# Kernel tuning notes

Measured on AMD Instinct MI355X. Metric: run time of the kernel, lower is better.

## Reference

```python
import jax, jax.numpy as jnp
import numpy as np

N = 50000
E = 800000
N_IN = 256
N_HID = 128
N_OUT = 64
HOP = 10


def setup_inputs() -> dict:
    key = jax.random.key(0)
    ks = jax.random.split(key, 12)
    x = jax.random.normal(ks[0], (N, N_IN), dtype=jnp.float32)
    s = jax.random.randint(ks[1], (E,), 0, N, dtype=jnp.int32)
    t = jax.random.randint(ks[2], (E,), 0, N, dtype=jnp.int32)
    # parameters (xavier-ish scaling)
    fc1W = jax.random.normal(ks[3], (N_HID, N_IN), dtype=jnp.float32) * (1.0 / np.sqrt(N_IN))
    fc1b = jnp.zeros((N_HID,), dtype=jnp.float32)
    fcsW = jax.random.normal(ks[4], (HOP, N_HID, N_HID), dtype=jnp.float32) * (1.0 / np.sqrt(N_HID))
    fcsb = jnp.zeros((HOP, N_HID), dtype=jnp.float32)
    a1 = jax.random.normal(ks[5], (HOP, N_HID), dtype=jnp.float32) * (1.0 / np.sqrt(N_HID))
    a2 = jax.random.normal(ks[6], (HOP, N_HID), dtype=jnp.float32) * (1.0 / np.sqrt(N_HID))
    fc2W = jax.random.normal(ks[7], (N_OUT, N_HID), dtype=jnp.float32) * (1.0 / np.sqrt(N_HID))
    fc2b = jnp.zeros((N_OUT,), dtype=jnp.float32)
    return {"x": x, "s": s, "t": t, "fc1W": fc1W, "fc1b": fc1b,
            "fcsW": fcsW, "fcsb": fcsb, "a1": a1, "a2": a2,
            "fc2W": fc2W, "fc2b": fc2b}


def reference(x, s, t, fc1W, fc1b, fcsW, fcsb, a1, a2, fc2W, fc2b):
    # dropout layers are identity in eval mode
    x = jax.nn.relu(x @ fc1W.T + fc1b)  # [N, n_hid]
    h = x
    for i in range(HOP):
        W, b = fcsW[i], fcsb[i]
        x_new = x @ W.T + b          # [N, n_hid]
        h = h @ W.T + b              # [N, n_hid]
        x1 = x_new @ a1[i]           # [N]
        h1 = h @ a2[i]               # [N]
        w1 = jnp.exp(jax.nn.leaky_relu(x1[s] + h1[t], 0.2))       # [E]
        w2 = jnp.exp(jax.nn.leaky_relu(x1 + x_new @ a2[i], 0.2))  # [N]
        div = jax.ops.segment_sum(w1, s, num_segments=N) + w2     # [N]
        num = jax.ops.segment_sum(w1[:, None] * h[t], s, num_segments=N) + w2[:, None] * x_new
        h = jax.nn.elu(num / div[:, None])
    return h @ fc2W.T + fc2b  # [N, n_out]
```

## Files before the change

kernel.cpp:

```cpp
#include <hip/hip_runtime.h>
#include <math.h>


typedef __attribute__((ext_vector_type(8))) short short8;
typedef __attribute__((ext_vector_type(4))) float f32x4;
#define MFMA16 __builtin_amdgcn_mfma_f32_16x16x32_bf16

__device__ __forceinline__ float lrelu02(float v) { return v > 0.f ? v : 0.2f * v; }

__device__ __forceinline__ float2 bf2f2(unsigned int v) {
    return make_float2(__uint_as_float(v << 16), __uint_as_float(v & 0xffff0000u));
}
__device__ __forceinline__ unsigned int f2bf(float f) {
    unsigned int u = __float_as_uint(f);
    u += 0x7fffu + ((u >> 16) & 1u);
    return u >> 16;
}
__device__ __forceinline__ float hi_part(float f) {
    return __uint_as_float(__float_as_uint(f) & 0xffff0000u);
}
__device__ __forceinline__ uint4 pack_hi(const float4& a, const float4& b) {
    uint4 r;
    r.x = (__float_as_uint(a.x) >> 16) | (__float_as_uint(a.y) & 0xffff0000u);
    r.y = (__float_as_uint(a.z) >> 16) | (__float_as_uint(a.w) & 0xffff0000u);
    r.z = (__float_as_uint(b.x) >> 16) | (__float_as_uint(b.y) & 0xffff0000u);
    r.w = (__float_as_uint(b.z) >> 16) | (__float_as_uint(b.w) & 0xffff0000u);
    return r;
}
__device__ __forceinline__ uint4 pack_lo(const float4& a, const float4& b) {
    uint4 r;
    r.x = f2bf(a.x - hi_part(a.x)) | (f2bf(a.y - hi_part(a.y)) << 16);
    r.y = f2bf(a.z - hi_part(a.z)) | (f2bf(a.w - hi_part(a.w)) << 16);
    r.z = f2bf(b.x - hi_part(b.x)) | (f2bf(b.y - hi_part(b.y)) << 16);
    r.w = f2bf(b.z - hi_part(b.z)) | (f2bf(b.w - hi_part(b.w)) << 16);
    return r;
}

__global__ __launch_bounds__(256) void k_count(const int* __restrict__ s, int* __restrict__ cnt, int E) {
    int e = blockIdx.x * 256 + threadIdx.x;
    if (e < E) atomicAdd(&cnt[s[e]], 1);
}

__global__ __launch_bounds__(256) void k_scan1(const int* __restrict__ cnt, int* __restrict__ bs, int N) {
    __shared__ int sh[256];
    int idx = blockIdx.x * 256 + threadIdx.x;
    sh[threadIdx.x] = (idx < N) ? cnt[idx] : 0;
    __syncthreads();
#pragma unroll
    for (int off = 128; off; off >>= 1) {
        if (threadIdx.x < off) sh[threadIdx.x] += sh[threadIdx.x + off];
        __syncthreads();
    }
    if (threadIdx.x == 0) bs[blockIdx.x] = sh[0];
}

__global__ __launch_bounds__(256) void k_scan2(int* __restrict__ bs, int G) {
    __shared__ int sh[256];
    int t = threadIdx.x;
    int v = (t < G) ? bs[t] : 0;
    sh[t] = v;
    __syncthreads();
    int val = v;
#pragma unroll
    for (int off = 1; off < 256; off <<= 1) {
        int o = (t >= off) ? sh[t - off] : 0;
        __syncthreads();
        val += o; sh[t] = val;
        __syncthreads();
    }
    if (t < G) bs[t] = val - v;
}

__global__ __launch_bounds__(256) void k_scan3(const int* __restrict__ cnt, const int* __restrict__ bs,
                                               int* __restrict__ rp, int N) {
    __shared__ int sh[256];
    int t = threadIdx.x;
    int idx = blockIdx.x * 256 + t;
    int v = (idx < N) ? cnt[idx] : 0;
    sh[t] = v;
    __syncthreads();
    int val = v;
#pragma unroll
    for (int off = 1; off < 256; off <<= 1) {
        int o = (t >= off) ? sh[t - off] : 0;
        __syncthreads();
        val += o; sh[t] = val;
        __syncthreads();
    }
    if (idx <= N) rp[idx] = val - v + bs[blockIdx.x];
}

__global__ __launch_bounds__(256) void k_scatter(const int* __restrict__ s, const int* __restrict__ t,
                                                 const int* __restrict__ rp, int* __restrict__ cursor,
                                                 int* __restrict__ t_sorted, int E) {
    int e = blockIdx.x * 256 + threadIdx.x;
    if (e < E) {
        int u = s[e];
        int pos = atomicAdd(&cursor[u], 1);
        t_sorted[rp[u] + pos] = t[e];
    }
}

__global__ __launch_bounds__(256) void k_wsplit(const float* __restrict__ W,
                                                unsigned short* __restrict__ Whi,
                                                unsigned short* __restrict__ Wlo, int total) {
    int i = blockIdx.x * 256 + threadIdx.x;
    if (i < total) {
        float f = W[i];
        unsigned int u = __float_as_uint(f);
        Whi[i] = (unsigned short)(u >> 16);
        Wlo[i] = (unsigned short)f2bf(f - __uint_as_float(u & 0xffff0000u));
    }
}

__global__ __launch_bounds__(256) void k_fc1(
    const float* __restrict__ Xf,
    const unsigned short* __restrict__ Wh, const unsigned short* __restrict__ Wl,
    const float* __restrict__ bias,
    unsigned short* __restrict__ Yhi, unsigned short* __restrict__ Ylo, int N) {
    const int tid = threadIdx.x;
    const int r0 = blockIdx.x * 128;
    const int lane = tid & 63;
    const int w = tid >> 6;
    const int wr = (w >> 1) * 64, wc = (w & 1) * 64;
    const int frow = lane & 15;
    const int fk = lane >> 4;
    const int q4 = lane >> 4;

    f32x4 acc[4][4];
#pragma unroll
    for (int i = 0; i < 4; ++i)
#pragma unroll
        for (int j = 0; j < 4; ++j) acc[i][j] = (f32x4){0.f, 0.f, 0.f, 0.f};

    const float4 z4 = make_float4(0.f, 0.f, 0.f, 0.f);
#pragma unroll
    for (int kc = 0; kc < 8; ++kc) {
        short8 ah[4], al[4];
#pragma unroll
        for (int ri = 0; ri < 4; ++ri) {
            int row = r0 + wr + ri * 16 + frow;
            float4 va = z4, vb = z4;
            if (row < N) {
                const float* p = Xf + (size_t)row * 256 + kc * 32 + fk * 8;
                va = *(const float4*)p;
                vb = *(const float4*)(p + 4);
            }
            uint4 h = pack_hi(va, vb);
            uint4 l = pack_lo(va, vb);
            ah[ri] = *(short8*)&h;
            al[ri] = *(short8*)&l;
        }
#pragma unroll
        for (int ci = 0; ci < 4; ++ci) {
            int col = wc + ci * 16 + frow;
            short8 bh = *(const short8*)(Wh + (size_t)col * 256 + kc * 32 + fk * 8);
            short8 bl = *(const short8*)(Wl + (size_t)col * 256 + kc * 32 + fk * 8);
#pragma unroll
            for (int ri = 0; ri < 4; ++ri) {
                acc[ri][ci] = MFMA16(ah[ri], bh, acc[ri][ci], 0, 0, 0);
                acc[ri][ci] = MFMA16(ah[ri], bl, acc[ri][ci], 0, 0, 0);
                acc[ri][ci] = MFMA16(al[ri], bh, acc[ri][ci], 0, 0, 0);
            }
        }
    }

#pragma unroll
    for (int ci = 0; ci < 4; ++ci) {
        int col = wc + ci * 16 + frow;
        float bcol = bias[col];
#pragma unroll
        for (int ri = 0; ri < 4; ++ri) {
            f32x4 v = acc[ri][ci];
#pragma unroll
            for (int reg = 0; reg < 4; ++reg) {
                int grow = r0 + wr + ri * 16 + q4 * 4 + reg;
                if (grow < N) {
                    float val = fmaxf(v[reg] + bcol, 0.f);
                    Yhi[(size_t)grow * 128 + col] = (unsigned short)(__float_as_uint(val) >> 16);
                    Ylo[(size_t)grow * 128 + col] = (unsigned short)f2bf(val - hi_part(val));
                }
            }
        }
    }
}

__global__ __launch_bounds__(256) void k_fc2(
    const unsigned short* __restrict__ Xhi,
    const unsigned short* __restrict__ Wh, const unsigned short* __restrict__ Wl,
    const float* __restrict__ bias, float* __restrict__ Yf, int N) {
    const int tid = threadIdx.x;
    const int r0 = blockIdx.x * 64;
    const int lane = tid & 63;
    const int w = tid >> 6;
    const int wr = w * 16;
    const int frow = lane & 15;
    const int fk = lane >> 4;
    const int q4 = lane >> 4;

    f32x4 acc[4];
#pragma unroll
    for (int j = 0; j < 4; ++j) acc[j] = (f32x4){0.f, 0.f, 0.f, 0.f};

    const short8 z8 = (short8){0, 0, 0, 0, 0, 0, 0, 0};
#pragma unroll
    for (int kc = 0; kc < 4; ++kc) {
        int row = r0 + wr + frow;
        short8 ah = (row < N) ? *(const short8*)(Xhi + (size_t)row * 128 + kc * 32 + fk * 8) : z8;
#pragma unroll
        for (int ci = 0; ci < 4; ++ci) {
            int col = ci * 16 + frow;
            short8 bh = *(const short8*)(Wh + (size_t)col * 128 + kc * 32 + fk * 8);
            short8 bl = *(const short8*)(Wl + (size_t)col * 128 + kc * 32 + fk * 8);
            acc[ci] = MFMA16(ah, bh, acc[ci], 0, 0, 0);
            acc[ci] = MFMA16(ah, bl, acc[ci], 0, 0, 0);
        }
    }

#pragma unroll
    for (int ci = 0; ci < 4; ++ci) {
        int col = ci * 16 + frow;
        float bcol = bias[col];
#pragma unroll
        for (int reg = 0; reg < 4; ++reg) {
            int grow = r0 + wr + q4 * 4 + reg;
            if (grow < N) Yf[(size_t)grow * 64 + col] = acc[ci][reg] + bcol;
        }
    }
}

__global__ __launch_bounds__(256) void k_mm_bf(
    const unsigned short* __restrict__ Xhi0, const unsigned short* __restrict__ Xlo0, int nblk0,
    const unsigned short* __restrict__ Hhi1,
    const unsigned short* __restrict__ Whi, const unsigned short* __restrict__ Wlo,
    const float* __restrict__ bias,
    unsigned short* __restrict__ Yb0, unsigned short* __restrict__ Yb1, int N,
    const float* __restrict__ dA0, float* __restrict__ oA0,
    const float* __restrict__ dB0, float* __restrict__ oB0,
    const float* __restrict__ dA1, float* __restrict__ oA1) {
    __shared__ unsigned short lds[2 * 128 * 128];

    const int tid = threadIdx.x;
    const bool second = (int)blockIdx.x >= nblk0;
    const int bx = second ? (int)blockIdx.x - nblk0 : (int)blockIdx.x;
    const int r0 = bx * 128;

    {
        int col = tid & 127;
        int pl = tid >> 7;
        const unsigned short* wp = (pl ? Wlo : Whi) + (size_t)col * 128;
        unsigned short* dst = lds + pl * 16384 + col * 128;
#pragma unroll
        for (int g = 0; g < 16; ++g)
            *(uint4*)(dst + ((g ^ (col & 7)) * 8)) = ((const uint4*)wp)[g];
    }
    __syncthreads();

    const int lane = tid & 63;
    const int w = tid >> 6;
    const int wr = (w >> 1) * 64, wc = (w & 1) * 64;
    const int frow = lane & 15;
    const int fk = lane >> 4;
    const int q4 = lane >> 4;

    const unsigned short* Xh = second ? Hhi1 : Xhi0;
    const unsigned short* Xl = Xlo0;
    unsigned short* Yb = second ? Yb1 : Yb0;

    f32x4 acc[4][4];
#pragma unroll
    for (int i = 0; i < 4; ++i)
#pragma unroll
        for (int j = 0; j < 4; ++j) acc[i][j] = (f32x4){0.f, 0.f, 0.f, 0.f};

    const short8 z8 = (short8){0, 0, 0, 0, 0, 0, 0, 0};

#pragma unroll
    for (int kc = 0; kc < 4; ++kc) {
        short8 ah[4], al[4], bh[4], bl[4];
#pragma unroll
        for (int ri = 0; ri < 4; ++ri) {
            int row = r0 + wr + ri * 16 + frow;
            bool ok = row < N;
            const unsigned short* ph = Xh + (size_t)row * 128 + kc * 32 + fk * 8;
            ah[ri] = ok ? *(const short8*)ph : z8;
            if (!second) {
                const unsigned short* pl = Xl + (size_t)row * 128 + kc * 32 + fk * 8;
                al[ri] = ok ? *(const short8*)pl : z8;
            }
        }
#pragma unroll
        for (int ci = 0; ci < 4; ++ci) {
            int col = wc + ci * 16 + frow;
            int g = kc * 4 + fk;
            int go = (g ^ (col & 7)) * 8;
            bh[ci] = *(const short8*)(lds + col * 128 + go);
            bl[ci] = *(const short8*)(lds + 16384 + col * 128 + go);
        }
        if (!second) {
#pragma unroll
            for (int ri = 0; ri < 4; ++ri)
#pragma unroll
                for (int ci = 0; ci < 4; ++ci) {
                    acc[ri][ci] = MFMA16(ah[ri], bh[ci], acc[ri][ci], 0, 0, 0);
                    acc[ri][ci] = MFMA16(ah[ri], bl[ci], acc[ri][ci], 0, 0, 0);
                    acc[ri][ci] = MFMA16(al[ri], bh[ci], acc[ri][ci], 0, 0, 0);
                }
        } else {
#pragma unroll
            for (int ri = 0; ri < 4; ++ri)
#pragma unroll
                for (int ci = 0; ci < 4; ++ci) {
                    acc[ri][ci] = MFMA16(ah[ri], bh[ci], acc[ri][ci], 0, 0, 0);
                    acc[ri][ci] = MFMA16(ah[ri], bl[ci], acc[ri][ci], 0, 0, 0);
                }
        }
    }

    const float* dA = second ? dA1 : dA0;
    const float* dB = second ? nullptr : dB0;
    unsigned short* So = lds;
    float* dotbuf = (float*)(lds + 16384);

    float dotA[4][4] = {}, dotB[4][4] = {};
    __syncthreads();
#pragma unroll
    for (int ci = 0; ci < 4; ++ci) {
        int col = wc + ci * 16 + frow;
        float bcol = bias[col];
        float dAc = dA ? dA[col] : 0.f;
        float dBc = dB ? dB[col] : 0.f;
#pragma unroll
        for (int ri = 0; ri < 4; ++ri) {
            f32x4 v = acc[ri][ci];
#pragma unroll
            for (int reg = 0; reg < 4; ++reg) {
                float val = v[reg] + bcol;
                int row = wr + ri * 16 + q4 * 4 + reg;
                int dw = (col >> 1) ^ ((row & 12) << 1);
                So[row * 128 + dw * 2 + (col & 1)] = (unsigned short)f2bf(val);
                dotA[ri][reg] = fmaf(val, dAc, dotA[ri][reg]);
                dotB[ri][reg] = fmaf(val, dBc, dotB[ri][reg]);
            }
        }
    }
#pragma unroll
    for (int m = 1; m < 16; m <<= 1)
#pragma unroll
        for (int ri = 0; ri < 4; ++ri)
#pragma unroll
            for (int reg = 0; reg < 4; ++reg) {
                dotA[ri][reg] += __shfl_xor(dotA[ri][reg], m, 64);
                dotB[ri][reg] += __shfl_xor(dotB[ri][reg], m, 64);
            }
    if (frow == 0) {
#pragma unroll
        for (int ri = 0; ri < 4; ++ri)
#pragma unroll
            for (int reg = 0; reg < 4; ++reg) {
                int rl = wr + ri * 16 + q4 * 4 + reg;
                dotbuf[(0 * 128 + rl) * 2 + (w & 1)] = dotA[ri][reg];
                dotbuf[(1 * 128 + rl) * 2 + (w & 1)] = dotB[ri][reg];
            }
    }
    __syncthreads();

#pragma unroll
    for (int q = 0; q < 8; ++q) {
        int idx = q * 256 + tid;
        int row = idx >> 4;
        int gc = idx & 15;
        int dwb = (gc * 4) ^ ((row & 12) << 1);
        uint4 vv = *(const uint4*)(So + row * 128 + dwb * 2);
        int grow = r0 + row;
        if (grow < N) *(uint4*)(Yb + (size_t)grow * 128 + gc * 8) = vv;
    }
    {
        int d = tid >> 7, rl = tid & 127;
        int grow = r0 + rl;
        float* oA = second ? oA1 : oA0;
        float* oB = second ? nullptr : oB0;
        if (grow < N) {
            float v = dotbuf[(d * 128 + rl) * 2] + dotbuf[(d * 128 + rl) * 2 + 1];
            if (d == 0) { if (oA) oA[grow] = v; }
            else        { if (oB) oB[grow] = v; }
        }
    }
}

__global__ __launch_bounds__(256) void k_agg(
    const unsigned short* __restrict__ xnb, const unsigned short* __restrict__ hbf,
    const float* __restrict__ x1a, const float* __restrict__ xa2a,
    const float* __restrict__ h1a, const int* __restrict__ rp,
    const int* __restrict__ ts,
    unsigned short* __restrict__ hhi, int N) {
    __shared__ uint2 ew[4][64];
    const int wid = threadIdx.x >> 6;
    const int lane = threadIdx.x & 63;
    const int u = blockIdx.x * 4 + wid;
    if (u >= N) return;
    const int l2 = lane << 1;
    float x1u = x1a[u];
    float w2 = expf(lrelu02(x1u + xa2a[u]));
    float2 xr = bf2f2(*(const unsigned int*)(xnb + (size_t)u * 128 + l2));
    float accx = w2 * xr.x, accy = w2 * xr.y;
    float div = w2;
    int p0 = rp[u], p1 = rp[u + 1];
    for (int base = p0; base < p1; base += 64) {
        int e = base + lane;
        uint2 pk = make_uint2(0u, 0u);
        if (e < p1) {
            int tv = ts[e];
            pk.x = (unsigned int)tv;
            pk.y = __float_as_uint(expf(lrelu02(x1u + h1a[tv])));
        }
        ew[wid][lane] = pk;
        int m = p1 - base; if (m > 64) m = 64;
        int m8 = (m + 7) & ~7;
        for (int j = 0; j < m8; j += 8) {
            uint2 q[8];
#pragma unroll
            for (int k = 0; k < 8; ++k) q[k] = ew[wid][j + k];
            unsigned int hv[8];
#pragma unroll
            for (int k = 0; k < 8; ++k)
                hv[k] = *(const unsigned int*)(hbf + (size_t)q[k].x * 128 + l2);
#pragma unroll
            for (int k = 0; k < 8; ++k) {
                float ww = __uint_as_float(q[k].y);
                float2 f = bf2f2(hv[k]);
                accx = fmaf(ww, f.x, accx);
                accy = fmaf(ww, f.y, accy);
                div += ww;
            }
        }
    }
    float ox = accx / div, oy = accy / div;
    ox = ox > 0.f ? ox : expf(ox) - 1.f;
    oy = oy > 0.f ? oy : expf(oy) - 1.f;
    unsigned int hx = __float_as_uint(ox), hy = __float_as_uint(oy);
    *(unsigned int*)(hhi + (size_t)u * 128 + l2) = (hx >> 16) | (hy & 0xffff0000u);
}

extern "C" void kernel_launch(void* const* d_in, const int* in_sizes, int n_in,
                              void* d_out, int out_size, void* d_ws, size_t ws_size,
                              hipStream_t stream) {
    const float* x_in = (const float*)d_in[0];
    const int*   s    = (const int*)d_in[1];
    const int*   t    = (const int*)d_in[2];
    const float* fc1W = (const float*)d_in[3];
    const float* fc1b = (const float*)d_in[4];
    const float* fcsW = (const float*)d_in[5];
    const float* fcsb = (const float*)d_in[6];
    const float* a1   = (const float*)d_in[7];
    const float* a2   = (const float*)d_in[8];
    const float* fc2W = (const float*)d_in[9];
    const float* fc2b = (const float*)d_in[10];

    const int N = in_sizes[0] / 256;
    const int E = in_sizes[1];
    const int G = (N + 255) / 256;
    const int NB = (N + 127) / 128;

    char* ws = (char*)d_ws;
    size_t off = 0;
    auto alloc = [&](size_t bytes) -> void* {
        void* p = ws + off;
        off += (bytes + 255) & ~(size_t)255;
        return p;
    };
    unsigned short* xbuf_hi = (unsigned short*)alloc((size_t)N * 128 * 2);
    unsigned short* xbuf_lo = (unsigned short*)alloc((size_t)N * 128 * 2);
    unsigned short* h_hi    = (unsigned short*)alloc((size_t)N * 128 * 2);
    unsigned short* xnb     = (unsigned short*)alloc((size_t)N * 128 * 2);
    unsigned short* hbf     = (unsigned short*)alloc((size_t)N * 128 * 2);
    unsigned short* Whi  = (unsigned short*)alloc((size_t)10 * 128 * 128 * 2);
    unsigned short* Wlo  = (unsigned short*)alloc((size_t)10 * 128 * 128 * 2);
    unsigned short* W1hi = (unsigned short*)alloc((size_t)128 * 256 * 2);
    unsigned short* W1lo = (unsigned short*)alloc((size_t)128 * 256 * 2);
    unsigned short* W2hi = (unsigned short*)alloc((size_t)64 * 128 * 2);
    unsigned short* W2lo = (unsigned short*)alloc((size_t)64 * 128 * 2);
    float* x1a  = (float*)alloc((size_t)N * 4);
    float* xa2a = (float*)alloc((size_t)N * 4);
    float* h1a  = (float*)alloc((size_t)N * 4);
    int* row_ptr  = (int*)alloc((size_t)(N + 1) * 4);
    int* cnt      = (int*)alloc((size_t)N * 4);
    int* bsums    = (int*)alloc((size_t)256 * 4);
    int* t_sorted = (int*)alloc((size_t)E * 4);

    hipMemsetAsync(cnt, 0, (size_t)N * 4, stream);
    k_count<<<(E + 255) / 256, 256, 0, stream>>>(s, cnt, E);
    k_scan1<<<G, 256, 0, stream>>>(cnt, bsums, N);
    k_scan2<<<1, 256, 0, stream>>>(bsums, G);
    k_scan3<<<G, 256, 0, stream>>>(cnt, bsums, row_ptr, N);
    hipMemsetAsync(cnt, 0, (size_t)N * 4, stream);
    k_scatter<<<(E + 255) / 256, 256, 0, stream>>>(s, t, row_ptr, cnt, t_sorted, E);

    k_wsplit<<<(10 * 128 * 128 + 255) / 256, 256, 0, stream>>>(fcsW, Whi, Wlo, 10 * 128 * 128);
    k_wsplit<<<(128 * 256 + 255) / 256, 256, 0, stream>>>(fc1W, W1hi, W1lo, 128 * 256);
    k_wsplit<<<(64 * 128 + 255) / 256, 256, 0, stream>>>(fc2W, W2hi, W2lo, 64 * 128);

    k_fc1<<<NB, 256, 0, stream>>>(x_in, W1hi, W1lo, fc1b, xbuf_hi, xbuf_lo, N);

    for (int i = 0; i < 10; ++i) {
        const unsigned short* Wh = Whi + (size_t)i * 128 * 128;
        const unsigned short* Wl = Wlo + (size_t)i * 128 * 128;
        const float* b   = fcsb + (size_t)i * 128;
        const float* a1i = a1 + (size_t)i * 128;
        const float* a2i = a2 + (size_t)i * 128;
        if (i == 0) {
            k_mm_bf<<<NB, 256, 0, stream>>>(xbuf_hi, xbuf_lo, NB, h_hi,
                                            Wh, Wl, b, xnb, hbf, N,
                                            a1i, x1a, a2i, xa2a, a2i, h1a);
            k_agg<<<(N + 3) / 4, 256, 0, stream>>>(xnb, xnb, x1a, xa2a, xa2a,
                                                   row_ptr, t_sorted, h_hi, N);
        } else {
            k_mm_bf<<<2 * NB, 256, 0, stream>>>(xbuf_hi, xbuf_lo, NB, h_hi,
                                                Wh, Wl, b, xnb, hbf, N,
                                                a1i, x1a, a2i, xa2a, a2i, h1a);
            k_agg<<<(N + 3) / 4, 256, 0, stream>>>(xnb, hbf, x1a, xa2a, h1a,
                                                   row_ptr, t_sorted, h_hi, N);
        }
    }

    k_fc2<<<(N + 63) / 64, 256, 0, stream>>>(h_hi, W2hi, W2lo, fc2b, (float*)d_out, N);
}
```

Before: 859.5 us.

## Batch all hop x-side projections into one launch and split h-side GEMM

Result: no change. 851.6 us (-0.9%).

```diff
diff --git a/kernel.cpp b/kernel.cpp
--- a/kernel.cpp
+++ b/kernel.cpp
@@ -119,26 +119,26 @@
     const float* __restrict__ bias,
     unsigned short* __restrict__ Yhi, unsigned short* __restrict__ Ylo, int N) {
     const int tid = threadIdx.x;
-    const int r0 = blockIdx.x * 128;
+    const int r0 = blockIdx.x * 64;
     const int lane = tid & 63;
     const int w = tid >> 6;
-    const int wr = (w >> 1) * 64, wc = (w & 1) * 64;
+    const int wr = (w >> 1) * 32, wc = (w & 1) * 64;
     const int frow = lane & 15;
     const int fk = lane >> 4;
     const int q4 = lane >> 4;
 
-    f32x4 acc[4][4];
-#pragma unroll
-    for (int i = 0; i < 4; ++i)
+    f32x4 acc[2][4];
+#pragma unroll
+    for (int i = 0; i < 2; ++i)
 #pragma unroll
         for (int j = 0; j < 4; ++j) acc[i][j] = (f32x4){0.f, 0.f, 0.f, 0.f};
 
     const float4 z4 = make_float4(0.f, 0.f, 0.f, 0.f);
 #pragma unroll
     for (int kc = 0; kc < 8; ++kc) {
-        short8 ah[4], al[4];
-#pragma unroll
-        for (int ri = 0; ri < 4; ++ri) {
+        short8 ah[2], al[2];
+#pragma unroll
+        for (int ri = 0; ri < 2; ++ri) {
             int row = r0 + wr + ri * 16 + frow;
             float4 va = z4, vb = z4;
             if (row < N) {
@@ -157,7 +157,7 @@
             short8 bh = *(const short8*)(Wh + (size_t)col * 256 + kc * 32 + fk * 8);
             short8 bl = *(const short8*)(Wl + (size_t)col * 256 + kc * 32 + fk * 8);
 #pragma unroll
-            for (int ri = 0; ri < 4; ++ri) {
+            for (int ri = 0; ri < 2; ++ri) {
                 acc[ri][ci] = MFMA16(ah[ri], bh, acc[ri][ci], 0, 0, 0);
                 acc[ri][ci] = MFMA16(ah[ri], bl, acc[ri][ci], 0, 0, 0);
                 acc[ri][ci] = MFMA16(al[ri], bh, acc[ri][ci], 0, 0, 0);
@@ -170,7 +170,7 @@
         int col = wc + ci * 16 + frow;
         float bcol = bias[col];
 #pragma unroll
-        for (int ri = 0; ri < 4; ++ri) {
+        for (int ri = 0; ri < 2; ++ri) {
             f32x4 v = acc[ri][ci];
 #pragma unroll
             for (int reg = 0; reg < 4; ++reg) {
@@ -229,26 +229,32 @@
     }
 }
 
-__global__ __launch_bounds__(256) void k_mm_bf(
-    const unsigned short* __restrict__ Xhi0, const unsigned short* __restrict__ Xlo0, int nblk0,
-    const unsigned short* __restrict__ Hhi1,
-    const unsigned short* __restrict__ Whi, const unsigned short* __restrict__ Wlo,
-    const float* __restrict__ bias,
-    unsigned short* __restrict__ Yb0, unsigned short* __restrict__ Yb1, int N,
-    const float* __restrict__ dA0, float* __restrict__ oA0,
-    const float* __restrict__ dB0, float* __restrict__ oB0,
-    const float* __restrict__ dA1, float* __restrict__ oA1) {
+__global__ __launch_bounds__(256) void k_xall(
+    const unsigned short* __restrict__ Xhi, const unsigned short* __restrict__ Xlo, int NB,
+    const unsigned short* __restrict__ Whi_all, const unsigned short* __restrict__ Wlo_all,
+    const float* __restrict__ fcsb, const float* __restrict__ a1, const float* __restrict__ a2,
+    int i0, unsigned short* __restrict__ xnb_all,
+    float* __restrict__ x1a_all, float* __restrict__ xa2a_all, int N) {
     __shared__ unsigned short lds[2 * 128 * 128];
 
     const int tid = threadIdx.x;
-    const bool second = (int)blockIdx.x >= nblk0;
-    const int bx = second ? (int)blockIdx.x - nblk0 : (int)blockIdx.x;
+    const int islot = (int)blockIdx.x / NB;
+    const int bx = (int)blockIdx.x % NB;
+    const int ih = i0 + islot;
+    const unsigned short* Wh = Whi_all + (size_t)ih * 16384;
+    const unsigned short* Wl = Wlo_all + (size_t)ih * 16384;
+    const float* bias = fcsb + ih * 128;
+    const float* dA = a1 + ih * 128;
+    const float* dB = a2 + ih * 128;
+    unsigned short* Yb = xnb_all + (size_t)islot * N * 128;
+    float* oA = x1a_all + (size_t)islot * N;
+    float* oB = xa2a_all + (size_t)islot * N;
     const int r0 = bx * 128;
 
     {
         int col = tid & 127;
         int pl = tid >> 7;
-        const unsigned short* wp = (pl ? Wlo : Whi) + (size_t)col * 128;
+        const unsigned short* wp = (pl ? Wl : Wh) + (size_t)col * 128;
         unsigned short* dst = lds + pl * 16384 + col * 128;
 #pragma unroll
         for (int g = 0; g < 16; ++g)
@@ -263,10 +269,6 @@
     const int fk = lane >> 4;
     const int q4 = lane >> 4;
 
-    const unsigned short* Xh = second ? Hhi1 : Xhi0;
-    const unsigned short* Xl = Xlo0;
-    unsigned short* Yb = second ? Yb1 : Yb0;
-
     f32x4 acc[4][4];
 #pragma unroll
     for (int i = 0; i < 4; ++i)
@@ -282,12 +284,8 @@
         for (int ri = 0; ri < 4; ++ri) {
             int row = r0 + wr + ri * 16 + frow;
             bool ok = row < N;
-            const unsigned short* ph = Xh + (size_t)row * 128 + kc * 32 + fk * 8;
-            ah[ri] = ok ? *(const short8*)ph : z8;
-            if (!second) {
-                const unsigned short* pl = Xl + (size_t)row * 128 + kc * 32 + fk * 8;
-                al[ri] = ok ? *(const short8*)pl : z8;
-            }
+            ah[ri] = ok ? *(const short8*)(Xhi + (size_t)row * 128 + kc * 32 + fk * 8) : z8;
+            al[ri] = ok ? *(const short8*)(Xlo + (size_t)row * 128 + kc * 32 + fk * 8) : z8;
         }
 #pragma unroll
         for (int ci = 0; ci < 4; ++ci) {
@@ -297,28 +295,16 @@
             bh[ci] = *(const short8*)(lds + col * 128 + go);
             bl[ci] = *(const short8*)(lds + 16384 + col * 128 + go);
         }
-        if (!second) {
-#pragma unroll
-            for (int ri = 0; ri < 4; ++ri)
-#pragma unroll
-                for (int ci = 0; ci < 4; ++ci) {
-                    acc[ri][ci] = MFMA16(ah[ri], bh[ci], acc[ri][ci], 0, 0, 0);
-                    acc[ri][ci] = MFMA16(ah[ri], bl[ci], acc[ri][ci], 0, 0, 0);
-                    acc[ri][ci] = MFMA16(al[ri], bh[ci], acc[ri][ci], 0, 0, 0);
-                }
-        } else {
-#pragma unroll
-            for (int ri = 0; ri < 4; ++ri)
-#pragma unroll
-                for (int ci = 0; ci < 4; ++ci) {
-                    acc[ri][ci] = MFMA16(ah[ri], bh[ci], acc[ri][ci], 0, 0, 0);
-                    acc[ri][ci] = MFMA16(ah[ri], bl[ci], acc[ri][ci], 0, 0, 0);
-                }
-        }
-    }
-
-    const float* dA = second ? dA1 : dA0;
-    const float* dB = second ? nullptr : dB0;
+#pragma unroll
+        for (int ri = 0; ri < 4; ++ri)
+#pragma unroll
+            for (int ci = 0; ci < 4; ++ci) {
+                acc[ri][ci] = MFMA16(ah[ri], bh[ci], acc[ri][ci], 0, 0, 0);
+                acc[ri][ci] = MFMA16(ah[ri], bl[ci], acc[ri][ci], 0, 0, 0);
+                acc[ri][ci] = MFMA16(al[ri], bh[ci], acc[ri][ci], 0, 0, 0);
+            }
+    }
+
     unsigned short* So = lds;
     float* dotbuf = (float*)(lds + 16384);
 
@@ -328,8 +314,8 @@
     for (int ci = 0; ci < 4; ++ci) {
         int col = wc + ci * 16 + frow;
         float bcol = bias[col];
-        float dAc = dA ? dA[col] : 0.f;
-        float dBc = dB ? dB[col] : 0.f;
+        float dAc = dA[col];
+        float dBc = dB[col];
 #pragma unroll
         for (int ri = 0; ri < 4; ++ri) {
             f32x4 v = acc[ri][ci];
@@ -378,13 +364,108 @@
     {
         int d = tid >> 7, rl = tid & 127;
         int grow = r0 + rl;
-        float* oA = second ? oA1 : oA0;
-        float* oB = second ? nullptr : oB0;
         if (grow < N) {
             float v = dotbuf[(d * 128 + rl) * 2] + dotbuf[(d * 128 + rl) * 2 + 1];
-            if (d == 0) { if (oA) oA[grow] = v; }
-            else        { if (oB) oB[grow] = v; }
-        }
+            if (d == 0) oA[grow] = v;
+            else        oB[grow] = v;
+        }
+    }
+}
+
+__global__ __launch_bounds__(256) void k_hh(
+    const unsigned short* __restrict__ Hhi,
+    const unsigned short* __restrict__ Wh, const unsigned short* __restrict__ Wl,
+    const float* __restrict__ bias, const float* __restrict__ dA2,
+    unsigned short* __restrict__ hbf, float* __restrict__ h1a, int N) {
+    __shared__ unsigned short So[64 * 128];
+    __shared__ float dotbuf[64][2];
+    const int tid = threadIdx.x;
+    const int r0 = blockIdx.x * 64;
+    const int lane = tid & 63;
+    const int w = tid >> 6;
+    const int wr = (w >> 1) * 32, wc = (w & 1) * 64;
+    const int frow = lane & 15;
+    const int fk = lane >> 4;
+    const int q4 = lane >> 4;
+
+    f32x4 acc[2][4];
+#pragma unroll
+    for (int i = 0; i < 2; ++i)
+#pragma unroll
+        for (int j = 0; j < 4; ++j) acc[i][j] = (f32x4){0.f, 0.f, 0.f, 0.f};
+
+    const short8 z8 = (short8){0, 0, 0, 0, 0, 0, 0, 0};
+#pragma unroll
+    for (int kc = 0; kc < 4; ++kc) {
+        short8 ah[2];
+#pragma unroll
+        for (int ri = 0; ri < 2; ++ri) {
+            int row = r0 + wr + ri * 16 + frow;
+            ah[ri] = (row < N) ? *(const short8*)(Hhi + (size_t)row * 128 + kc * 32 + fk * 8) : z8;
+        }
+#pragma unroll
+        for (int ci = 0; ci < 4; ++ci) {
+            int col = wc + ci * 16 + frow;
+            short8 bh = *(const short8*)(Wh + (size_t)col * 128 + kc * 32 + fk * 8);
+            short8 bl = *(const short8*)(Wl + (size_t)col * 128 + kc * 32 + fk * 8);
+#pragma unroll
+            for (int ri = 0; ri < 2; ++ri) {
+                acc[ri][ci] = MFMA16(ah[ri], bh, acc[ri][ci], 0, 0, 0);
+                acc[ri][ci] = MFMA16(ah[ri], bl, acc[ri][ci], 0, 0, 0);
+            }
+        }
+    }
+
+    float dotA[2][4] = {};
+#pragma unroll
+    for (int ci = 0; ci < 4; ++ci) {
+        int col = wc + ci * 16 + frow;
+        float bcol = bias[col];
+        float dAc = dA2[col];
+#pragma unroll
+        for (int ri = 0; ri < 2; ++ri) {
+            f32x4 v = acc[ri][ci];
+#pragma unroll
+            for (int reg = 0; reg < 4; ++reg) {
+                float val = v[reg] + bcol;
+                int row = wr + ri * 16 + q4 * 4 + reg;
+                int dw = (col >> 1) ^ ((row & 12) << 1);
+                So[row * 128 + dw * 2 + (col & 1)] = (unsigned short)f2bf(val);
+                dotA[ri][reg] = fmaf(val, dAc, dotA[ri][reg]);
+            }
+        }
+    }
+#pragma unroll
+    for (int m = 1; m < 16; m <<= 1)
+#pragma unroll
+        for (int ri = 0; ri < 2; ++ri)
+#pragma unroll
+            for (int reg = 0; reg < 4; ++reg)
+                dotA[ri][reg] += __shfl_xor(dotA[ri][reg], m, 64);
+    if (frow == 0) {
+#pragma unroll
+        for (int ri = 0; ri < 2; ++ri)
+#pragma unroll
+            for (int reg = 0; reg < 4; ++reg) {
+                int rl = wr + ri * 16 + q4 * 4 + reg;
+                dotbuf[rl][w & 1] = dotA[ri][reg];
+            }
+    }
+    __syncthreads();
+
+#pragma unroll
+    for (int q = 0; q < 4; ++q) {
+        int idx = q * 256 + tid;
+        int row = idx >> 4;
+        int gc = idx & 15;
+        int dwb = (gc * 4) ^ ((row & 12) << 1);
+        uint4 vv = *(const uint4*)(So + row * 128 + dwb * 2);
+        int grow = r0 + row;
+        if (grow < N) *(uint4*)(hbf + (size_t)grow * 128 + gc * 8) = vv;
+    }
+    if (tid < 64) {
+        int grow = r0 + tid;
+        if (grow < N) h1a[grow] = dotbuf[tid][0] + dotbuf[tid][1];
     }
 }
 
@@ -461,6 +542,18 @@
     const int E = in_sizes[1];
     const int G = (N + 255) / 256;
     const int NB = (N + 127) / 128;
+    const int NB64 = (N + 63) / 64;
+
+    auto A256 = [](size_t b) { return (b + 255) & ~(size_t)255; };
+    const size_t plane = A256((size_t)N * 128 * 2);
+    const size_t vecN  = A256((size_t)N * 4);
+    size_t fixed = 3 * plane
+                 + plane
+                 + 2 * A256((size_t)10 * 16384 * 2)
+                 + 2 * A256((size_t)128 * 256 * 2) + 2 * A256((size_t)64 * 128 * 2)
+                 + vecN
+                 + A256((size_t)(N + 1) * 4) + vecN + A256(1024) + A256((size_t)E * 4);
+    const int BATCH = (fixed + 10 * (plane + 2 * vecN) <= ws_size) ? 10 : 1;
 
     char* ws = (char*)d_ws;
     size_t off = 0;
@@ -472,21 +565,21 @@
     unsigned short* xbuf_hi = (unsigned short*)alloc((size_t)N * 128 * 2);
     unsigned short* xbuf_lo = (unsigned short*)alloc((size_t)N * 128 * 2);
     unsigned short* h_hi    = (unsigned short*)alloc((size_t)N * 128 * 2);
-    unsigned short* xnb     = (unsigned short*)alloc((size_t)N * 128 * 2);
     unsigned short* hbf     = (unsigned short*)alloc((size_t)N * 128 * 2);
-    unsigned short* Whi  = (unsigned short*)alloc((size_t)10 * 128 * 128 * 2);
-    unsigned short* Wlo  = (unsigned short*)alloc((size_t)10 * 128 * 128 * 2);
+    unsigned short* Whi  = (unsigned short*)alloc((size_t)10 * 16384 * 2);
+    unsigned short* Wlo  = (unsigned short*)alloc((size_t)10 * 16384 * 2);
     unsigned short* W1hi = (unsigned short*)alloc((size_t)128 * 256 * 2);
     unsigned short* W1lo = (unsigned short*)alloc((size_t)128 * 256 * 2);
     unsigned short* W2hi = (unsigned short*)alloc((size_t)64 * 128 * 2);
     unsigned short* W2lo = (unsigned short*)alloc((size_t)64 * 128 * 2);
-    float* x1a  = (float*)alloc((size_t)N * 4);
-    float* xa2a = (float*)alloc((size_t)N * 4);
     float* h1a  = (float*)alloc((size_t)N * 4);
     int* row_ptr  = (int*)alloc((size_t)(N + 1) * 4);
     int* cnt      = (int*)alloc((size_t)N * 4);
-    int* bsums    = (int*)alloc((size_t)256 * 4);
+    int* bsums    = (int*)alloc((size_t)1024);
     int* t_sorted = (int*)alloc((size_t)E * 4);
+    unsigned short* xnb_all = (unsigned short*)alloc((size_t)BATCH * N * 128 * 2);
+    float* x1a_all  = (float*)alloc((size_t)BATCH * N * 4);
+    float* xa2a_all = (float*)alloc((size_t)BATCH * N * 4);
 
     hipMemsetAsync(cnt, 0, (size_t)N * 4, stream);
     k_count<<<(E + 255) / 256, 256, 0, stream>>>(s, cnt, E);
@@ -496,32 +589,35 @@
     hipMemsetAsync(cnt, 0, (size_t)N * 4, stream);
     k_scatter<<<(E + 255) / 256, 256, 0, stream>>>(s, t, row_ptr, cnt, t_sorted, E);
 
-    k_wsplit<<<(10 * 128 * 128 + 255) / 256, 256, 0, stream>>>(fcsW, Whi, Wlo, 10 * 128 * 128);
+    k_wsplit<<<(10 * 16384 + 255) / 256, 256, 0, stream>>>(fcsW, Whi, Wlo, 10 * 16384);
     k_wsplit<<<(128 * 256 + 255) / 256, 256, 0, stream>>>(fc1W, W1hi, W1lo, 128 * 256);
     k_wsplit<<<(64 * 128 + 255) / 256, 256, 0, stream>>>(fc2W, W2hi, W2lo, 64 * 128);
 
-    k_fc1<<<NB, 256, 0, stream>>>(x_in, W1hi, W1lo, fc1b, xbuf_hi, xbuf_lo, N);
+    k_fc1<<<NB64, 256, 0, stream>>>(x_in, W1hi, W1lo, fc1b, xbuf_hi, xbuf_lo, N);
+
+    if (BATCH == 10)
+        k_xall<<<10 * NB, 256, 0, stream>>>(xbuf_hi, xbuf_lo, NB, Whi, Wlo,
+                                            fcsb, a1, a2, 0, xnb_all, x1a_all, xa2a_all, N);
 
     for (int i = 0; i < 10; ++i) {
-        const unsigned short* Wh = Whi + (size_t)i * 128 * 128;
-        const unsigned short* Wl = Wlo + (size_t)i * 128 * 128;
-        const float* b   = fcsb + (size_t)i * 128;
-        const float* a1i = a1 + (size_t)i * 128;
-        const float* a2i = a2 + (size_t)i * 128;
+        if (BATCH == 1)
+            k_xall<<<NB, 256, 0, stream>>>(xbuf_hi, xbuf_lo, NB, Whi, Wlo,
+                                           fcsb, a1, a2, i, xnb_all, x1a_all, xa2a_all, N);
+        const int sl = (BATCH == 10) ? i : 0;
+        const unsigned short* xnb_i = xnb_all + (size_t)sl * N * 128;
+        const float* x1_i  = x1a_all + (size_t)sl * N;
+        const float* xa2_i = xa2a_all + (size_t)sl * N;
         if (i == 0) {
-            k_mm_bf<<<NB, 256, 0, stream>>>(xbuf_hi, xbuf_lo, NB, h_hi,
-                                            Wh, Wl, b, xnb, hbf, N,
-                                            a1i, x1a, a2i, xa2a, a2i, h1a);
-            k_agg<<<(N + 3) / 4, 256, 0, stream>>>(xnb, xnb, x1a, xa2a, xa2a,
+            k_agg<<<(N + 3) / 4, 256, 0, stream>>>(xnb_i, xnb_i, x1_i, xa2_i, xa2_i,
                                                    row_ptr, t_sorted, h_hi, N);
         } else {
-            k_mm_bf<<<2 * NB, 256, 0, stream>>>(xbuf_hi, xbuf_lo, NB, h_hi,
-                                                Wh, Wl, b, xnb, hbf, N,
-                                                a1i, x1a, a2i, xa2a, a2i, h1a);
-            k_agg<<<(N + 3) / 4, 256, 0, stream>>>(xnb, hbf, x1a, xa2a, h1a,
+            k_hh<<<NB64, 256, 0, stream>>>(h_hi, Whi + (size_t)i * 16384, Wlo + (size_t)i * 16384,
+                                           fcsb + (size_t)i * 128, a2 + (size_t)i * 128,
+                                           hbf, h1a, N);
+            k_agg<<<(N + 3) / 4, 256, 0, stream>>>(xnb_i, hbf, x1_i, xa2_i, h1a,
                                                    row_ptr, t_sorted, h_hi, N);
         }
     }
 
-    k_fc2<<<(N + 63) / 64, 256, 0, stream>>>(h_hi, W2hi, W2lo, fc2b, (float*)d_out, N);
-}
+    k_fc2<<<NB64, 256, 0, stream>>>(h_hi, W2hi, W2lo, fc2b, (float*)d_out, N);
+}
```
